# Performance work log

Measured on AMD Instinct MI355X. Metric: run time of the kernel, lower is better.

## Reference

```python
import jax, jax.numpy as jnp
import numpy as np

N = 30000       # nodes
E = 480000      # edges (before self loops)
IN = 128        # in_channels
H1, C1 = 5, 64  # conv1 heads, per-head channels
OUT = 64        # out_channels (conv2, heads=1)
PE = 100000     # pos/neg edges for decode
NEG_SLOPE = 0.2


def setup_inputs() -> dict:
    key = jax.random.key(0)
    ks = jax.random.split(key, 12)
    return {
        "x": jax.random.normal(ks[0], (N, IN), dtype=jnp.float32),
        "edge_index": jax.random.randint(ks[1], (2, E), 0, N),
        "pos_edge_index": jax.random.randint(ks[2], (2, PE), 0, N),
        "neg_edge_index": jax.random.randint(ks[3], (2, PE), 0, N),
        "W1": jax.random.normal(ks[4], (IN, H1 * C1), dtype=jnp.float32) * 0.05,
        "att_src1": jax.random.normal(ks[5], (H1, C1), dtype=jnp.float32) * 0.1,
        "att_dst1": jax.random.normal(ks[6], (H1, C1), dtype=jnp.float32) * 0.1,
        "b1": jnp.zeros((H1 * C1,), dtype=jnp.float32),
        "W2": jax.random.normal(ks[7], (H1 * C1, OUT), dtype=jnp.float32) * 0.05,
        "att_src2": jax.random.normal(ks[8], (1, OUT), dtype=jnp.float32) * 0.1,
        "att_dst2": jax.random.normal(ks[9], (1, OUT), dtype=jnp.float32) * 0.1,
        "b2": jnp.zeros((OUT,), dtype=jnp.float32),
    }


def gat_conv(x, edge_index, W, att_src, att_dst, bias, heads, out_ch):
    """PyG GATConv: add self loops, linear proj, edge softmax, scatter-sum, concat heads."""
    n = x.shape[0]
    loops = jnp.arange(n)
    src = jnp.concatenate([edge_index[0], loops])  # message sources j
    dst = jnp.concatenate([edge_index[1], loops])  # message targets i
    h = (x @ W).reshape(n, heads, out_ch)          # [N,H,C]
    a_src = jnp.sum(h * att_src, axis=-1)          # [N,H]
    a_dst = jnp.sum(h * att_dst, axis=-1)          # [N,H]
    e = jax.nn.leaky_relu(a_src[src] + a_dst[dst], NEG_SLOPE)  # [E',H]
    # numerically-stable segment softmax over incoming edges of each dst node
    m = jax.ops.segment_max(e, dst, num_segments=n)
    m = jax.lax.stop_gradient(jnp.where(jnp.isfinite(m), m, 0.0))
    ex = jnp.exp(e - m[dst])
    s = jax.ops.segment_sum(ex, dst, num_segments=n)
    alpha = ex / (s[dst] + 1e-16)                  # [E',H]
    out = jax.ops.segment_sum(alpha[:, :, None] * h[src], dst, num_segments=n)  # [N,H,C]
    return out.reshape(n, heads * out_ch) + bias


def reference(x, edge_index, pos_edge_index, neg_edge_index,
              W1, att_src1, att_dst1, b1, W2, att_src2, att_dst2, b2):
    z = gat_conv(x, edge_index, W1, att_src1, att_dst1, b1, H1, C1)
    z = jax.nn.relu(z)
    z = gat_conv(z, edge_index, W2, att_src2, att_dst2, b2, 1, OUT)
    ei = jnp.concatenate([pos_edge_index, neg_edge_index], axis=-1)
    return jnp.sum(z[ei[0]] * z[ei[1]], axis=-1)  # [2*PE]
```

## Files before the change

kernel.cpp:

```cpp
#include <hip/hip_runtime.h>
#include <hip/hip_fp16.h>
#include <cstdint>
#include <cstddef>
#include <type_traits>

#define N_NODES 30000
#define N_EDGES 480000
#define N_EDGES_SL (N_EDGES + N_NODES)
#define IN_CH 128
#define HEADS1 5
#define C1 64
#define D1 (HEADS1 * C1)
#define OUT_CH 64
#define PE_CNT 100000
#define NEG_SLOPE 0.2f
#define BCAP 64

typedef _Float16 f16x8 __attribute__((ext_vector_type(8)));
typedef _Float16 f16x2 __attribute__((ext_vector_type(2)));
typedef float fx4 __attribute__((ext_vector_type(4)));

#if defined(__has_builtin)
#if __has_builtin(__builtin_amdgcn_fdot2)
#define HAS_FDOT2 1
#endif
#endif

static __device__ __forceinline__ float leaky(float x) {
    return x > 0.f ? x : NEG_SLOPE * x;
}

template<int NH, typename AT>
static __device__ __forceinline__ void gemm_phase(const AT* __restrict__ A,
                                                  const __half* __restrict__ Wt,
                                                  __half* __restrict__ C, int K,
                                                  const float* __restrict__ att_src,
                                                  const float* __restrict__ att_dst,
                                                  float* __restrict__ as_out,
                                                  float* __restrict__ ad_out,
                                                  int slot, int nsl, int lane) {
    const int N = NH * 64;
    int q = lane >> 4, l16 = lane & 15;
    for (int tile = slot; tile < N_NODES / 16; tile += nsl) {
        int rowBase = tile * 16;
        int arow = rowBase + l16;
        fx4 zero4 = {0.f, 0.f, 0.f, 0.f};
        fx4 acc[NH][4];
#pragma unroll
        for (int h = 0; h < NH; ++h)
#pragma unroll
            for (int c = 0; c < 4; ++c) acc[h][c] = zero4;
        for (int kk = 0; kk < K; kk += 32) {
            f16x8 af;
            if constexpr (std::is_same<AT, float>::value) {
                const float4* s = (const float4*)(A + (size_t)arow * K + kk + q * 8);
                float4 v0 = s[0], v1 = s[1];
                af[0] = (_Float16)v0.x; af[1] = (_Float16)v0.y;
                af[2] = (_Float16)v0.z; af[3] = (_Float16)v0.w;
                af[4] = (_Float16)v1.x; af[5] = (_Float16)v1.y;
                af[6] = (_Float16)v1.z; af[7] = (_Float16)v1.w;
            } else {
                af = *(const f16x8*)((const __half*)A + (size_t)arow * K + kk + q * 8);
            }
#pragma unroll
            for (int h = 0; h < NH; ++h) {
#pragma unroll
                for (int c = 0; c < 4; ++c) {
                    int col = h * 64 + c * 16 + l16;
                    f16x8 bf = *(const f16x8*)(Wt + (size_t)col * K + kk + q * 8);
                    acc[h][c] = __builtin_amdgcn_mfma_f32_16x16x32_f16(af, bf, acc[h][c], 0, 0, 0);
                }
            }
        }
#pragma unroll
        for (int h = 0; h < NH; ++h) {
            float ps[4] = {0.f, 0.f, 0.f, 0.f};
            float pd[4] = {0.f, 0.f, 0.f, 0.f};
#pragma unroll
            for (int c = 0; c < 4; ++c) {
                int gcol = h * 64 + c * 16 + l16;
                float av = att_src[gcol];
                float dv = att_dst[gcol];
#pragma unroll
                for (int reg = 0; reg < 4; ++reg) {
                    int grow = rowBase + q * 4 + reg;
                    float val = acc[h][c][reg];
                    C[(size_t)grow * N + gcol] = __float2half(val);
                    ps[reg] += val * av;
                    pd[reg] += val * dv;
                }
            }
#pragma unroll
            for (int off = 1; off < 16; off <<= 1) {
#pragma unroll
                for (int reg = 0; reg < 4; ++reg) {
                    ps[reg] += __shfl_xor(ps[reg], off, 64);
                    pd[reg] += __shfl_xor(pd[reg], off, 64);
                }
            }
            if (l16 == 0) {
#pragma unroll
                for (int reg = 0; reg < 4; ++reg) {
                    int grow = rowBase + q * 4 + reg;
                    as_out[(size_t)h * N_NODES + grow] = ps[reg];
                    ad_out[(size_t)h * N_NODES + grow] = pd[reg];
                }
            }
        }
    }
}

__global__ __launch_bounds__(256) void k_bucket_prep(const int* __restrict__ edge,
                                                     int* __restrict__ cnt,
                                                     int* __restrict__ esrc2,
                                                     int* __restrict__ ovf_cnt,
                                                     int* __restrict__ ovf,
                                                     const float* __restrict__ W1,
                                                     __half* __restrict__ Wt1,
                                                     const float* __restrict__ W2,
                                                     __half* __restrict__ Wt2) {
    int t = blockIdx.x * 256 + threadIdx.x;
    int nthr = gridDim.x * 256;
    for (int e = t; e < N_EDGES_SL; e += nthr) {
        int s, d;
        if (e < N_EDGES) { s = edge[e]; d = edge[N_EDGES + e]; }
        else { s = e - N_EDGES; d = s; }
        int r = atomicAdd(&cnt[d], 1);
        if (r < BCAP) {
            esrc2[d * BCAP + r] = s;
        } else {
            int oi = atomicAdd(ovf_cnt, 1);
            ovf[2 * oi] = d;
            ovf[2 * oi + 1] = s;
        }
    }
    const int T1 = IN_CH * D1, T2 = D1 * OUT_CH;
    for (int idx = t; idx < T1 + T2; idx += nthr) {
        if (idx < T1) {
            int k = idx / D1, n = idx - k * D1;
            Wt1[(size_t)n * IN_CH + k] = __float2half(W1[idx]);
        } else {
            int i2 = idx - T1;
            int k = i2 / OUT_CH, n = i2 - k * OUT_CH;
            Wt2[(size_t)n * D1 + k] = __float2half(W2[i2]);
        }
    }
}

__global__ __launch_bounds__(256) void k_gemm1(const float* __restrict__ x,
                                               const __half* __restrict__ Wt1,
                                               __half* __restrict__ h1,
                                               const float* __restrict__ att_src1,
                                               const float* __restrict__ att_dst1,
                                               float* __restrict__ as1,
                                               float* __restrict__ ad1) {
    int lane = threadIdx.x & 63, wv = threadIdx.x >> 6;
    gemm_phase<HEADS1, float>(x, Wt1, h1, IN_CH, att_src1, att_dst1, as1, ad1,
                              blockIdx.x * 4 + wv, gridDim.x * 4, lane);
}

template<int NH, bool RELU>
__global__ __launch_bounds__(256) void k_attn_agg(const int* __restrict__ cnt,
                                                  const int* __restrict__ esrc2,
                                                  const int* __restrict__ ovf_cnt,
                                                  const int* __restrict__ ovf,
                                                  const __half* __restrict__ hf,
                                                  const float* __restrict__ a_src,
                                                  const float* __restrict__ a_dst,
                                                  const float* __restrict__ bias,
                                                  __half* __restrict__ zout) {
    __shared__ unsigned wpk[4][64];
    __shared__ int jbuf[4][64];
    int wid = (blockIdx.x * 256 + threadIdx.x) >> 6;
    int lane = threadIdx.x & 63;
    int wv = threadIdx.x >> 6;
    if (wid >= N_NODES * NH) return;
    int h = wid / N_NODES;
    int node = wid - h * N_NODES;
    int deg = cnt[node];
    const float* asrc_h = a_src + (size_t)h * N_NODES;
    float adst = a_dst[(size_t)h * N_NODES + node];
    const int RS = NH * 64;
    if (deg <= BCAP) {
        int es = lane >> 3, cg = lane & 7;
        const __half* hbase = hf + h * 64 + cg * 8;
        int j = 0;
        float ex = 0.f;
        if (lane < deg) {
            j = esrc2[node * BCAP + lane];
            ex = __expf(leaky(asrc_h[j] + adst));
        }
        float s = ex;
#pragma unroll
        for (int off = 1; off < 64; off <<= 1)
            s += __shfl_xor(s, off, 64);
        float r = 1.f / (s + 1e-16f);
        __half2 wn = __float2half2_rn(ex * r);
        wpk[wv][lane] = *(unsigned*)&wn;
        jbuf[wv][lane] = j;
        __half2 acch[4] = {__half2{0, 0}, __half2{0, 0}, __half2{0, 0}, __half2{0, 0}};
        for (int k0 = 0; k0 < deg; k0 += 32) {
            int kA = k0 + es, kB = k0 + 8 + es, kC = k0 + 16 + es, kD = k0 + 24 + es;
            bool oA = kA < deg, oB = kB < deg, oC = kC < deg, oD = kD < deg;
            unsigned uA = oA ? wpk[wv][kA] : 0u;
            unsigned uB = oB ? wpk[wv][kB] : 0u;
            unsigned uC = oC ? wpk[wv][kC] : 0u;
            unsigned uD = oD ? wpk[wv][kD] : 0u;
            int jA = jbuf[wv][oA ? kA : 0];
            int jB = jbuf[wv][oB ? kB : 0];
            int jC = jbuf[wv][oC ? kC : 0];
            int jD = jbuf[wv][oD ? kD : 0];
            float4 vA = *(const float4*)(hbase + (size_t)jA * RS);
            float4 vB = *(const float4*)(hbase + (size_t)jB * RS);
            float4 vC = *(const float4*)(hbase + (size_t)jC * RS);
            float4 vD = *(const float4*)(hbase + (size_t)jD * RS);
            __half2 hwA = *(__half2*)&uA, hwB = *(__half2*)&uB;
            __half2 hwC = *(__half2*)&uC, hwD = *(__half2*)&uD;
            const __half2* pA = (const __half2*)&vA;
            const __half2* pB = (const __half2*)&vB;
            const __half2* pC = (const __half2*)&vC;
            const __half2* pD = (const __half2*)&vD;
#pragma unroll
            for (int i = 0; i < 4; ++i) {
                acch[i] = __hfma2(pA[i], hwA, acch[i]);
                acch[i] = __hfma2(pB[i], hwB, acch[i]);
                acch[i] = __hfma2(pC[i], hwC, acch[i]);
                acch[i] = __hfma2(pD[i], hwD, acch[i]);
            }
        }
        float accf[8];
#pragma unroll
        for (int i = 0; i < 4; ++i) {
            float2 f = __half22float2(acch[i]);
            accf[2 * i] = f.x;
            accf[2 * i + 1] = f.y;
        }
#pragma unroll
        for (int m = 8; m < 64; m <<= 1)
#pragma unroll
            for (int i = 0; i < 8; ++i)
                accf[i] += __shfl_xor(accf[i], m, 64);
        if (es == 0) {
            const float* bb = bias + h * 64 + cg * 8;
            union { float4 f; __half2 hh[4]; } pk;
#pragma unroll
            for (int i = 0; i < 4; ++i) {
                float lo = accf[2 * i] + bb[2 * i];
                float hi = accf[2 * i + 1] + bb[2 * i + 1];
                if (RELU) { lo = fmaxf(lo, 0.f); hi = fmaxf(hi, 0.f); }
                pk.hh[i] = __floats2half2_rn(lo, hi);
            }
            *(float4*)(zout + (size_t)node * RS + h * 64 + cg * 8) = pk.f;
        }
    } else {
        int ovn = *ovf_cnt;
        int jb = esrc2[node * BCAP + lane];
        float s = __expf(leaky(asrc_h[jb] + adst));
#pragma unroll
        for (int off = 1; off < 64; off <<= 1)
            s += __shfl_xor(s, off, 64);
        float s2 = 0.f;
        for (int k = lane; k < ovn; k += 64)
            if (ovf[2 * k] == node)
                s2 += __expf(leaky(asrc_h[ovf[2 * k + 1]] + adst));
#pragma unroll
        for (int off = 1; off < 64; off <<= 1)
            s2 += __shfl_xor(s2, off, 64);
        float r = 1.f / (s + s2 + 1e-16f);
        float a = 0.f;
        for (int k = 0; k < BCAP; ++k) {
            int j = esrc2[node * BCAP + k];
            float w = __expf(leaky(asrc_h[j] + adst));
            a += w * __half2float(hf[(size_t)j * RS + h * 64 + lane]);
        }
        for (int k = 0; k < ovn; ++k) {
            if (ovf[2 * k] == node) {
                int j = ovf[2 * k + 1];
                float w = __expf(leaky(asrc_h[j] + adst));
                a += w * __half2float(hf[(size_t)j * RS + h * 64 + lane]);
            }
        }
        float o = a * r + bias[h * 64 + lane];
        if (RELU) o = fmaxf(o, 0.f);
        zout[(size_t)node * RS + h * 64 + lane] = __float2half(o);
    }
}

__global__ __launch_bounds__(256) void k_gemm2(const __half* __restrict__ z1,
                                               const __half* __restrict__ Wt2,
                                               __half* __restrict__ h2,
                                               const float* __restrict__ att_src2,
                                               const float* __restrict__ att_dst2,
                                               float* __restrict__ as2,
                                               float* __restrict__ ad2) {
    int lane = threadIdx.x & 63, wv = threadIdx.x >> 6;
    gemm_phase<1, __half>(z1, Wt2, h2, D1, att_src2, att_dst2, as2, ad2,
                          blockIdx.x * 4 + wv, gridDim.x * 4, lane);
}

__global__ __launch_bounds__(256) void k_decode(const int* __restrict__ pos,
                                                const int* __restrict__ neg,
                                                const __half* __restrict__ z2,
                                                float* __restrict__ out) {
    int t = blockIdx.x * 256 + threadIdx.x;
    int e = t >> 3;
    int lc = t & 7;
    if (e >= 2 * PE_CNT) return;
    int a, b;
    if (e < PE_CNT) { a = pos[e]; b = pos[PE_CNT + e]; }
    else { int k = e - PE_CNT; a = neg[k]; b = neg[PE_CNT + k]; }
    union U { float4 f; f16x2 h[4]; __half2 hh[4]; } ua, ub;
    ua.f = *(const float4*)(z2 + (size_t)a * OUT_CH + lc * 8);
    ub.f = *(const float4*)(z2 + (size_t)b * OUT_CH + lc * 8);
    float v = 0.f;
#pragma unroll
    for (int i = 0; i < 4; ++i) {
#ifdef HAS_FDOT2
        v = __builtin_amdgcn_fdot2(ua.h[i], ub.h[i], v, false);
#else
        float2 fa = __half22float2(ua.hh[i]);
        float2 fb = __half22float2(ub.hh[i]);
        v += fa.x * fb.x + fa.y * fb.y;
#endif
    }
#pragma unroll
    for (int off = 1; off < 8; off <<= 1)
        v += __shfl_xor(v, off, 64);
    if (lc == 0) out[e] = v;
}

extern "C" void kernel_launch(void* const* d_in, const int* in_sizes, int n_in,
                              void* d_out, int out_size, void* d_ws, size_t ws_size,
                              hipStream_t stream) {
    const float* x        = (const float*)d_in[0];
    const int* edge_index = (const int*)d_in[1];
    const int* pos_ei     = (const int*)d_in[2];
    const int* neg_ei     = (const int*)d_in[3];
    const float* W1       = (const float*)d_in[4];
    const float* att_src1 = (const float*)d_in[5];
    const float* att_dst1 = (const float*)d_in[6];
    const float* b1       = (const float*)d_in[7];
    const float* W2       = (const float*)d_in[8];
    const float* att_src2 = (const float*)d_in[9];
    const float* att_dst2 = (const float*)d_in[10];
    const float* b2       = (const float*)d_in[11];
    float* out            = (float*)d_out;

    char* ws = (char*)d_ws;
    size_t off = 0;
    auto alloc = [&](size_t bytes) -> void* {
        void* p = ws + off;
        off = (off + bytes + 255) & ~(size_t)255;
        return p;
    };
    int* cnt     = (int*)alloc(sizeof(int) * (N_NODES + 8));
    int* ovfc    = cnt + N_NODES;
    int* esrc2   = (int*)alloc(sizeof(int) * (size_t)N_NODES * BCAP);
    int* ovf     = (int*)alloc(sizeof(int) * (size_t)2 * N_EDGES_SL);
    __half* h1   = (__half*)alloc(sizeof(__half) * (size_t)N_NODES * D1);
    __half* z1   = (__half*)alloc(sizeof(__half) * (size_t)N_NODES * D1);
    __half* h2   = (__half*)alloc(sizeof(__half) * (size_t)N_NODES * OUT_CH);
    __half* z2   = (__half*)alloc(sizeof(__half) * (size_t)N_NODES * OUT_CH);
    __half* Wt1  = (__half*)alloc(sizeof(__half) * (size_t)D1 * IN_CH);
    __half* Wt2  = (__half*)alloc(sizeof(__half) * (size_t)OUT_CH * D1);
    float* as1   = (float*)alloc(sizeof(float) * (size_t)N_NODES * HEADS1);
    float* ad1   = (float*)alloc(sizeof(float) * (size_t)N_NODES * HEADS1);
    float* as2   = (float*)alloc(sizeof(float) * (size_t)N_NODES);
    float* ad2   = (float*)alloc(sizeof(float) * (size_t)N_NODES);

    hipMemsetAsync(cnt, 0, sizeof(int) * (N_NODES + 8), stream);
    k_bucket_prep<<<512, 256, 0, stream>>>(edge_index, cnt, esrc2, ovfc, ovf,
                                           W1, Wt1, W2, Wt2);
    k_gemm1<<<469, 256, 0, stream>>>(x, Wt1, h1, att_src1, att_dst1, as1, ad1);
    k_attn_agg<HEADS1, true><<<(N_NODES * HEADS1 + 3) / 4, 256, 0, stream>>>(
        cnt, esrc2, ovfc, ovf, h1, as1, ad1, b1, z1);
    k_gemm2<<<469, 256, 0, stream>>>(z1, Wt2, h2, att_src2, att_dst2, as2, ad2);
    k_attn_agg<1, false><<<(N_NODES + 3) / 4, 256, 0, stream>>>(
        cnt, esrc2, ovfc, ovf, h2, as2, ad2, b2, z2);
    k_decode<<<(2 * PE_CNT * 8 + 255) / 256, 256, 0, stream>>>(pos_ei, neg_ei, z2, out);

    (void)in_sizes; (void)n_in; (void)out_size; (void)ws_size;
}
```

Measured before the change: 251.3 us.

## Overlap edge bucketing with GEMM1 and reduce aggregation via shared memory

The hipMemsetAsync is replaced by a small init kernel that zeroes the counters and converts the weights. Edge bucketing now runs in extra blocks of the GEMM1 launch, so the atomic scatter overlaps the dense projection instead of being its own launch. The attention aggregation replaces the cross-lane shuffle reduction with a padded shared-memory transpose-and-sum, and each lane writes one half value. The trade-offs are extra LDS use per block, which may lower occupancy, and narrower scalar stores in place of float4 writes.

Result: faster. 213.2 us (-15.2%).

```diff
diff --git a/kernel.cpp b/kernel.cpp
--- a/kernel.cpp
+++ b/kernel.cpp
@@ -15,6 +15,8 @@
 #define PE_CNT 100000
 #define NEG_SLOPE 0.2f
 #define BCAP 64
+#define GEMM1_BLOCKS 469
+#define BUCKET_BLOCKS 128
 
 typedef _Float16 f16x8 __attribute__((ext_vector_type(8)));
 typedef _Float16 f16x2 __attribute__((ext_vector_type(2)));
@@ -110,30 +112,14 @@
     }
 }
 
-__global__ __launch_bounds__(256) void k_bucket_prep(const int* __restrict__ edge,
-                                                     int* __restrict__ cnt,
-                                                     int* __restrict__ esrc2,
-                                                     int* __restrict__ ovf_cnt,
-                                                     int* __restrict__ ovf,
-                                                     const float* __restrict__ W1,
-                                                     __half* __restrict__ Wt1,
-                                                     const float* __restrict__ W2,
-                                                     __half* __restrict__ Wt2) {
+__global__ __launch_bounds__(256) void k_init(int* __restrict__ cnt,
+                                              const float* __restrict__ W1,
+                                              __half* __restrict__ Wt1,
+                                              const float* __restrict__ W2,
+                                              __half* __restrict__ Wt2) {
     int t = blockIdx.x * 256 + threadIdx.x;
     int nthr = gridDim.x * 256;
-    for (int e = t; e < N_EDGES_SL; e += nthr) {
-        int s, d;
-        if (e < N_EDGES) { s = edge[e]; d = edge[N_EDGES + e]; }
-        else { s = e - N_EDGES; d = s; }
-        int r = atomicAdd(&cnt[d], 1);
-        if (r < BCAP) {
-            esrc2[d * BCAP + r] = s;
-        } else {
-            int oi = atomicAdd(ovf_cnt, 1);
-            ovf[2 * oi] = d;
-            ovf[2 * oi + 1] = s;
-        }
-    }
+    for (int i = t; i < N_NODES + 8; i += nthr) cnt[i] = 0;
     const int T1 = IN_CH * D1, T2 = D1 * OUT_CH;
     for (int idx = t; idx < T1 + T2; idx += nthr) {
         if (idx < T1) {
@@ -147,16 +133,39 @@
     }
 }
 
-__global__ __launch_bounds__(256) void k_gemm1(const float* __restrict__ x,
-                                               const __half* __restrict__ Wt1,
-                                               __half* __restrict__ h1,
-                                               const float* __restrict__ att_src1,
-                                               const float* __restrict__ att_dst1,
-                                               float* __restrict__ as1,
-                                               float* __restrict__ ad1) {
+__global__ __launch_bounds__(256) void k_build_gemm1(const int* __restrict__ edge,
+                                                     int* __restrict__ cnt,
+                                                     int* __restrict__ esrc2,
+                                                     int* __restrict__ ovf_cnt,
+                                                     int* __restrict__ ovf,
+                                                     const float* __restrict__ x,
+                                                     const __half* __restrict__ Wt1,
+                                                     __half* __restrict__ h1,
+                                                     const float* __restrict__ att_src1,
+                                                     const float* __restrict__ att_dst1,
+                                                     float* __restrict__ as1,
+                                                     float* __restrict__ ad1) {
     int lane = threadIdx.x & 63, wv = threadIdx.x >> 6;
-    gemm_phase<HEADS1, float>(x, Wt1, h1, IN_CH, att_src1, att_dst1, as1, ad1,
-                              blockIdx.x * 4 + wv, gridDim.x * 4, lane);
+    if (blockIdx.x < GEMM1_BLOCKS) {
+        gemm_phase<HEADS1, float>(x, Wt1, h1, IN_CH, att_src1, att_dst1, as1, ad1,
+                                  blockIdx.x * 4 + wv, GEMM1_BLOCKS * 4, lane);
+    } else {
+        int t = (blockIdx.x - GEMM1_BLOCKS) * 256 + threadIdx.x;
+        int nthr = BUCKET_BLOCKS * 256;
+        for (int e = t; e < N_EDGES_SL; e += nthr) {
+            int s, d;
+            if (e < N_EDGES) { s = edge[e]; d = edge[N_EDGES + e]; }
+            else { s = e - N_EDGES; d = s; }
+            int r = atomicAdd(&cnt[d], 1);
+            if (r < BCAP) {
+                esrc2[d * BCAP + r] = s;
+            } else {
+                int oi = atomicAdd(ovf_cnt, 1);
+                ovf[2 * oi] = d;
+                ovf[2 * oi + 1] = s;
+            }
+        }
+    }
 }
 
 template<int NH, bool RELU>
@@ -171,6 +180,7 @@
                                                   __half* __restrict__ zout) {
     __shared__ unsigned wpk[4][64];
     __shared__ int jbuf[4][64];
+    __shared__ float red[4][584];
     int wid = (blockIdx.x * 256 + threadIdx.x) >> 6;
     int lane = threadIdx.x & 63;
     int wv = threadIdx.x >> 6;
@@ -228,30 +238,19 @@
                 acch[i] = __hfma2(pD[i], hwD, acch[i]);
             }
         }
-        float accf[8];
 #pragma unroll
         for (int i = 0; i < 4; ++i) {
             float2 f = __half22float2(acch[i]);
-            accf[2 * i] = f.x;
-            accf[2 * i + 1] = f.y;
-        }
-#pragma unroll
-        for (int m = 8; m < 64; m <<= 1)
-#pragma unroll
-            for (int i = 0; i < 8; ++i)
-                accf[i] += __shfl_xor(accf[i], m, 64);
-        if (es == 0) {
-            const float* bb = bias + h * 64 + cg * 8;
-            union { float4 f; __half2 hh[4]; } pk;
-#pragma unroll
-            for (int i = 0; i < 4; ++i) {
-                float lo = accf[2 * i] + bb[2 * i];
-                float hi = accf[2 * i + 1] + bb[2 * i + 1];
-                if (RELU) { lo = fmaxf(lo, 0.f); hi = fmaxf(hi, 0.f); }
-                pk.hh[i] = __floats2half2_rn(lo, hi);
-            }
-            *(float4*)(zout + (size_t)node * RS + h * 64 + cg * 8) = pk.f;
-        }
+            red[wv][(cg * 8 + 2 * i) * 9 + es] = f.x;
+            red[wv][(cg * 8 + 2 * i + 1) * 9 + es] = f.y;
+        }
+        float tot = 0.f;
+#pragma unroll
+        for (int e2 = 0; e2 < 8; ++e2)
+            tot += red[wv][lane * 9 + e2];
+        float o = tot + bias[h * 64 + lane];
+        if (RELU) o = fmaxf(o, 0.f);
+        zout[(size_t)node * RS + h * 64 + lane] = __float2half(o);
     } else {
         int ovn = *ovf_cnt;
         int jb = esrc2[node * BCAP + lane];
@@ -368,10 +367,9 @@
     float* as2   = (float*)alloc(sizeof(float) * (size_t)N_NODES);
     float* ad2   = (float*)alloc(sizeof(float) * (size_t)N_NODES);
 
-    hipMemsetAsync(cnt, 0, sizeof(int) * (N_NODES + 8), stream);
-    k_bucket_prep<<<512, 256, 0, stream>>>(edge_index, cnt, esrc2, ovfc, ovf,
-                                           W1, Wt1, W2, Wt2);
-    k_gemm1<<<469, 256, 0, stream>>>(x, Wt1, h1, att_src1, att_dst1, as1, ad1);
+    k_init<<<240, 256, 0, stream>>>(cnt, W1, Wt1, W2, Wt2);
+    k_build_gemm1<<<GEMM1_BLOCKS + BUCKET_BLOCKS, 256, 0, stream>>>(
+        edge_index, cnt, esrc2, ovfc, ovf, x, Wt1, h1, att_src1, att_dst1, as1, ad1);
     k_attn_agg<HEADS1, true><<<(N_NODES * HEADS1 + 3) / 4, 256, 0, stream>>>(
         cnt, esrc2, ovfc, ovf, h1, as1, ad1, b1, z1);
     k_gemm2<<<469, 256, 0, stream>>>(z1, Wt2, h2, att_src2, att_dst2, as2, ad2);
```
